# Performance work log

Hardware: AMD Instinct MI355X
Metric: run time of the kernel (lower is better)

Reference implementation:

```python
import jax, jax.numpy as jnp
import numpy as np

B, H, L, D = 4, 16, 8192, 64


def setup_inputs() -> dict:
    key = jax.random.key(0)
    ks = jax.random.split(key, 10)
    q = jax.random.normal(ks[0], (B, H, L, D), dtype=jnp.float32)
    k = jax.random.normal(ks[1], (B, H, L, D), dtype=jnp.float32)
    v = jax.random.normal(ks[2], (B, H, L, D), dtype=jnp.float32)
    mask = jax.random.randint(ks[3], (B, H, L), 0, 2, dtype=jnp.int32)
    s = 1.0 / np.sqrt(D)
    Wa_w = jax.random.uniform(ks[4], (D, D), jnp.float32, -s, s)  # torch Linear weight [out,in]
    Wa_b = jax.random.uniform(ks[5], (D,), jnp.float32, -s, s)
    Ua_w = jax.random.uniform(ks[6], (D, D), jnp.float32, -s, s)
    Ua_b = jax.random.uniform(ks[7], (D,), jnp.float32, -s, s)
    va_w = jax.random.uniform(ks[8], (1, D), jnp.float32, -s, s)
    va_b = jax.random.uniform(ks[9], (1,), jnp.float32, -s, s)
    return {"q": q, "k": k, "v": v, "mask": mask,
            "Wa_w": Wa_w, "Wa_b": Wa_b, "Ua_w": Ua_w, "Ua_b": Ua_b,
            "va_w": va_w, "va_b": va_b}


def reference(q, k, v, mask, Wa_w, Wa_b, Ua_w, Ua_b, va_w, va_b):
    # e1 = Wa(q), e2 = Ua(k)  (torch Linear: x @ W.T + b)
    e1 = jnp.einsum('bhld,ed->bhle', q, Wa_w) + Wa_b
    e2 = jnp.einsum('bhld,ed->bhle', k, Ua_w) + Ua_b
    t = jnp.tanh(e1 + e2)
    # va: [B,H,L,D] -> [B,H,L]
    e = jnp.einsum('bhld,d->bhl', t, va_w[0]) + va_b[0]
    e = jnp.where(mask == 0, jnp.float32(-10000.0), e)
    alpha = jax.nn.softmax(e, axis=-1)  # softmax over sequence length
    return alpha[..., None] * v
```

## Files before the change

### kernel.cpp

```cpp
#include <hip/hip_runtime.h>
#include <hip/hip_bf16.h>

#define BH   64
#define LSEQ 8192
#define DDIM 64
#define NPOS (BH * LSEQ)
#define NT4  (NPOS * DDIM / 4)

typedef __attribute__((ext_vector_type(8))) short bf16x8;
typedef __attribute__((ext_vector_type(4))) float f32x4;

__device__ inline short f2bf(float f) {
    unsigned u = __builtin_bit_cast(unsigned, f);
    unsigned r = (u + 0x7FFFu + ((u >> 16) & 1u)) >> 16;
    return (short)r;
}
__device__ inline float bf2f(short s) {
    unsigned u = ((unsigned)(unsigned short)s) << 16;
    return __builtin_bit_cast(float, u);
}
__device__ inline void split8(const float* f, bf16x8& hi, bf16x8& lo) {
#pragma unroll
    for (int j = 0; j < 8; j++) {
        short h = f2bf(f[j]);
        hi[j] = h;
        lo[j] = f2bf(f[j] - bf2f(h));
    }
}
__device__ inline float tanh_fast(float x) {
    float ex = __expf(2.f * x);
    return 1.f - 2.f * __builtin_amdgcn_rcpf(ex + 1.f);
}

__global__ __launch_bounds__(256) void score_kernel(
    const float* __restrict__ q, const float* __restrict__ k,
    const int*   __restrict__ mask,
    const float* __restrict__ Waw, const float* __restrict__ Wab,
    const float* __restrict__ Uaw, const float* __restrict__ Uab,
    const float* __restrict__ vaw, const float* __restrict__ vab_p,
    float* __restrict__ e_out)
{
    const int lane = threadIdx.x & 63;
    const int m    = lane & 15;
    const int quad = lane >> 4;
    const int wgl  = blockIdx.x * 4 + (threadIdx.x >> 6);
    const long t0  = (long)wgl * 4;

    bf16x8 bwa[4][2], bua[4][2];
    float bias_s[4], vav[4];
#pragma unroll
    for (int t = 0; t < 4; t++) {
        const int n = t * 16 + m;
        bias_s[t] = Wab[n] + Uab[n];
        vav[t]    = vaw[n];
#pragma unroll
        for (int s = 0; s < 2; s++) {
            const int k0 = s * 32 + quad * 8;
            const float4 wA = ((const float4*)(Waw + n * 64 + k0))[0];
            const float4 wB = ((const float4*)(Waw + n * 64 + k0))[1];
            const float4 uA = ((const float4*)(Uaw + n * 64 + k0))[0];
            const float4 uB = ((const float4*)(Uaw + n * 64 + k0))[1];
            float wf[8] = {wA.x, wA.y, wA.z, wA.w, wB.x, wB.y, wB.z, wB.w};
            float uf[8] = {uA.x, uA.y, uA.z, uA.w, uB.x, uB.y, uB.z, uB.w};
            bf16x8 wv, uv;
#pragma unroll
            for (int j = 0; j < 8; j++) { wv[j] = f2bf(wf[j]); uv[j] = f2bf(uf[j]); }
            bwa[t][s] = wv;
            bua[t][s] = uv;
        }
    }
    const float vab = vab_p[0];

    float4 A[8], B[8];
    int4 mkA, mkB;

    auto issue = [&](float4 (&buf)[8], int4& mk, long tile) {
        mk = ((const int4*)mask)[tile * 4 + quad];
        const size_t off = (size_t)(tile * 16 + m) * 64 + quad * 8;
        buf[0] = *((const float4*)(q + off));
        buf[1] = *((const float4*)(q + off + 4));
        buf[2] = *((const float4*)(k + off));
        buf[3] = *((const float4*)(k + off + 4));
        buf[4] = *((const float4*)(q + off + 32));
        buf[5] = *((const float4*)(q + off + 36));
        buf[6] = *((const float4*)(k + off + 32));
        buf[7] = *((const float4*)(k + off + 36));
    };

    auto compute = [&](const float4 (&buf)[8], const int4& mk, long tile) {
        f32x4 acc[4];
#pragma unroll
        for (int t = 0; t < 4; t++) acc[t] = (f32x4){0.f, 0.f, 0.f, 0.f};
#pragma unroll
        for (int s = 0; s < 2; s++) {
            const float4 qa = buf[s * 4 + 0], qb = buf[s * 4 + 1];
            const float4 ka = buf[s * 4 + 2], kb = buf[s * 4 + 3];
            float qf[8] = {qa.x, qa.y, qa.z, qa.w, qb.x, qb.y, qb.z, qb.w};
            float kf[8] = {ka.x, ka.y, ka.z, ka.w, kb.x, kb.y, kb.z, kb.w};
            bf16x8 qhi, qlo, khi, klo;
            split8(qf, qhi, qlo);
            split8(kf, khi, klo);
#pragma unroll
            for (int t = 0; t < 4; t++) {
                acc[t] = __builtin_amdgcn_mfma_f32_16x16x32_bf16(qhi, bwa[t][s], acc[t], 0, 0, 0);
                acc[t] = __builtin_amdgcn_mfma_f32_16x16x32_bf16(qlo, bwa[t][s], acc[t], 0, 0, 0);
                acc[t] = __builtin_amdgcn_mfma_f32_16x16x32_bf16(khi, bua[t][s], acc[t], 0, 0, 0);
                acc[t] = __builtin_amdgcn_mfma_f32_16x16x32_bf16(klo, bua[t][s], acc[t], 0, 0, 0);
            }
        }
        float c[4] = {0.f, 0.f, 0.f, 0.f};
#pragma unroll
        for (int t = 0; t < 4; t++) {
#pragma unroll
            for (int r = 0; r < 4; r++)
                c[r] += vav[t] * tanh_fast(acc[t][r] + bias_s[t]);
        }
#pragma unroll
        for (int r = 0; r < 4; r++) {
#pragma unroll
            for (int off2 = 1; off2 < 16; off2 <<= 1)
                c[r] += __shfl_xor(c[r], off2, 16);
        }
        if (m == 0) {
            float4 ev;
            ev.x = mk.x ? c[0] + vab : -10000.f;
            ev.y = mk.y ? c[1] + vab : -10000.f;
            ev.z = mk.z ? c[2] + vab : -10000.f;
            ev.w = mk.w ? c[3] + vab : -10000.f;
            *((float4*)(e_out + tile * 16 + quad * 4)) = ev;
        }
    };

    issue(A, mkA, t0 + 0);
    issue(B, mkB, t0 + 1);
    compute(A, mkA, t0 + 0);
    issue(A, mkA, t0 + 2);
    compute(B, mkB, t0 + 1);
    issue(B, mkB, t0 + 3);
    compute(A, mkA, t0 + 2);
    compute(B, mkB, t0 + 3);
}

__global__ __launch_bounds__(1024) void rowstat_kernel(
    const float* __restrict__ e, float* __restrict__ stats)
{
    const int row = blockIdx.x;
    const size_t base = (size_t)row * LSEQ;
    const int tid  = threadIdx.x;
    const int lane = tid & 63;
    const int wv   = tid >> 6;
    __shared__ float redmax[16];
    __shared__ float redsum[16];

    float4 e0 = ((const float4*)(e + base))[tid];
    float4 e1 = ((const float4*)(e + base))[1024 + tid];
    float em[8] = {e0.x, e0.y, e0.z, e0.w, e1.x, e1.y, e1.z, e1.w};

    float lm = em[0];
#pragma unroll
    for (int j = 1; j < 8; j++) lm = fmaxf(lm, em[j]);
#pragma unroll
    for (int off = 32; off >= 1; off >>= 1) lm = fmaxf(lm, __shfl_xor(lm, off, 64));
    if (lane == 0) redmax[wv] = lm;
    __syncthreads();
    float M = redmax[0];
#pragma unroll
    for (int i = 1; i < 16; i++) M = fmaxf(M, redmax[i]);

    float ls = 0.f;
#pragma unroll
    for (int j = 0; j < 8; j++) ls += __expf(em[j] - M);
#pragma unroll
    for (int off = 32; off >= 1; off >>= 1) ls += __shfl_xor(ls, off, 64);
    if (lane == 0) redsum[wv] = ls;
    __syncthreads();
    if (tid == 0) {
        float S = 0.f;
#pragma unroll
        for (int i = 0; i < 16; i++) S += redsum[i];
        stats[row * 2]     = M;
        stats[row * 2 + 1] = 1.f / S;
    }
}

__global__ __launch_bounds__(256) void scale_kernel(
    const float* __restrict__ v, const float* __restrict__ e,
    const float* __restrict__ stats, float* __restrict__ out)
{
    const size_t i0 = (size_t)blockIdx.x * 256 + threadIdx.x;
    const size_t i1 = i0 + (size_t)(NT4 / 2);

    float4 v0 = ((const float4*)v)[i0];
    float4 v1 = ((const float4*)v)[i1];
    const size_t p0 = i0 >> 4, p1 = i1 >> 4;
    float e0 = e[p0], e1 = e[p1];
    const size_t r0 = p0 >> 13, r1 = p1 >> 13;
    float M0 = stats[r0 * 2], I0 = stats[r0 * 2 + 1];
    float M1 = stats[r1 * 2], I1 = stats[r1 * 2 + 1];

    float a0 = __expf(e0 - M0) * I0;
    float a1 = __expf(e1 - M1) * I1;
    float4 o0 = make_float4(a0 * v0.x, a0 * v0.y, a0 * v0.z, a0 * v0.w);
    float4 o1 = make_float4(a1 * v1.x, a1 * v1.y, a1 * v1.z, a1 * v1.w);
    ((float4*)out)[i0] = o0;
    ((float4*)out)[i1] = o1;
}

extern "C" void kernel_launch(void* const* d_in, const int* in_sizes, int n_in,
                              void* d_out, int out_size, void* d_ws, size_t ws_size,
                              hipStream_t stream) {
    const float* q    = (const float*)d_in[0];
    const float* k    = (const float*)d_in[1];
    const float* v    = (const float*)d_in[2];
    const int*   mask = (const int*)d_in[3];
    const float* Waw  = (const float*)d_in[4];
    const float* Wab  = (const float*)d_in[5];
    const float* Uaw  = (const float*)d_in[6];
    const float* Uab  = (const float*)d_in[7];
    const float* vaw  = (const float*)d_in[8];
    const float* vab  = (const float*)d_in[9];
    float* out = (float*)d_out;

    float* e_buf = (float*)d_ws;
    float* stats = (float*)d_ws + NPOS;

    score_kernel<<<2048, 256, 0, stream>>>(q, k, mask, Waw, Wab, Uaw, Uab, vaw, vab, e_buf);
    rowstat_kernel<<<BH, 1024, 0, stream>>>(e_buf, stats);
    scale_kernel<<<NT4 / 2 / 256, 256, 0, stream>>>(v, e_buf, stats, out);
}
```

Before: 418.8 us.

## Reorder weight loads after tile prefetch, add occupancy hint, nontemporal scale kernel

```diff
diff --git a/kernel.cpp b/kernel.cpp
--- a/kernel.cpp
+++ b/kernel.cpp
@@ -11,9 +11,8 @@
 typedef __attribute__((ext_vector_type(4))) float f32x4;
 
 __device__ inline short f2bf(float f) {
-    unsigned u = __builtin_bit_cast(unsigned, f);
-    unsigned r = (u + 0x7FFFu + ((u >> 16) & 1u)) >> 16;
-    return (short)r;
+    __bf16 b = (__bf16)f;
+    return __builtin_bit_cast(short, b);
 }
 __device__ inline float bf2f(short s) {
     unsigned u = ((unsigned)(unsigned short)s) << 16;
@@ -32,7 +31,7 @@
     return 1.f - 2.f * __builtin_amdgcn_rcpf(ex + 1.f);
 }
 
-__global__ __launch_bounds__(256) void score_kernel(
+__global__ __launch_bounds__(256, 3) void score_kernel(
     const float* __restrict__ q, const float* __restrict__ k,
     const int*   __restrict__ mask,
     const float* __restrict__ Waw, const float* __restrict__ Wab,
@@ -48,28 +47,7 @@
 
     bf16x8 bwa[4][2], bua[4][2];
     float bias_s[4], vav[4];
-#pragma unroll
-    for (int t = 0; t < 4; t++) {
-        const int n = t * 16 + m;
-        bias_s[t] = Wab[n] + Uab[n];
-        vav[t]    = vaw[n];
-#pragma unroll
-        for (int s = 0; s < 2; s++) {
-            const int k0 = s * 32 + quad * 8;
-            const float4 wA = ((const float4*)(Waw + n * 64 + k0))[0];
-            const float4 wB = ((const float4*)(Waw + n * 64 + k0))[1];
-            const float4 uA = ((const float4*)(Uaw + n * 64 + k0))[0];
-            const float4 uB = ((const float4*)(Uaw + n * 64 + k0))[1];
-            float wf[8] = {wA.x, wA.y, wA.z, wA.w, wB.x, wB.y, wB.z, wB.w};
-            float uf[8] = {uA.x, uA.y, uA.z, uA.w, uB.x, uB.y, uB.z, uB.w};
-            bf16x8 wv, uv;
-#pragma unroll
-            for (int j = 0; j < 8; j++) { wv[j] = f2bf(wf[j]); uv[j] = f2bf(uf[j]); }
-            bwa[t][s] = wv;
-            bua[t][s] = uv;
-        }
-    }
-    const float vab = vab_p[0];
+    float vab;
 
     float4 A[8], B[8];
     int4 mkA, mkB;
@@ -87,6 +65,31 @@
         buf[7] = *((const float4*)(k + off + 36));
     };
 
+    auto load_weights = [&]() {
+#pragma unroll
+        for (int t = 0; t < 4; t++) {
+            const int n = t * 16 + m;
+            bias_s[t] = Wab[n] + Uab[n];
+            vav[t]    = vaw[n];
+#pragma unroll
+            for (int s = 0; s < 2; s++) {
+                const int k0 = s * 32 + quad * 8;
+                const float4 wA = ((const float4*)(Waw + n * 64 + k0))[0];
+                const float4 wB = ((const float4*)(Waw + n * 64 + k0))[1];
+                const float4 uA = ((const float4*)(Uaw + n * 64 + k0))[0];
+                const float4 uB = ((const float4*)(Uaw + n * 64 + k0))[1];
+                float wf[8] = {wA.x, wA.y, wA.z, wA.w, wB.x, wB.y, wB.z, wB.w};
+                float uf[8] = {uA.x, uA.y, uA.z, uA.w, uB.x, uB.y, uB.z, uB.w};
+                bf16x8 wv, uv;
+#pragma unroll
+                for (int j = 0; j < 8; j++) { wv[j] = f2bf(wf[j]); uv[j] = f2bf(uf[j]); }
+                bwa[t][s] = wv;
+                bua[t][s] = uv;
+            }
+        }
+        vab = vab_p[0];
+    };
+
     auto compute = [&](const float4 (&buf)[8], const int4& mk, long tile) {
         f32x4 acc[4];
 #pragma unroll
@@ -133,10 +136,15 @@
 
     issue(A, mkA, t0 + 0);
     issue(B, mkB, t0 + 1);
+    __builtin_amdgcn_sched_barrier(0);
+    load_weights();
+    __builtin_amdgcn_sched_barrier(0);
     compute(A, mkA, t0 + 0);
     issue(A, mkA, t0 + 2);
+    __builtin_amdgcn_sched_barrier(0);
     compute(B, mkB, t0 + 1);
     issue(B, mkB, t0 + 3);
+    __builtin_amdgcn_sched_barrier(0);
     compute(A, mkA, t0 + 2);
     compute(B, mkB, t0 + 3);
 }
@@ -187,23 +195,31 @@
     const float* __restrict__ v, const float* __restrict__ e,
     const float* __restrict__ stats, float* __restrict__ out)
 {
-    const size_t i0 = (size_t)blockIdx.x * 256 + threadIdx.x;
-    const size_t i1 = i0 + (size_t)(NT4 / 2);
-
-    float4 v0 = ((const float4*)v)[i0];
-    float4 v1 = ((const float4*)v)[i1];
-    const size_t p0 = i0 >> 4, p1 = i1 >> 4;
-    float e0 = e[p0], e1 = e[p1];
-    const size_t r0 = p0 >> 13, r1 = p1 >> 13;
-    float M0 = stats[r0 * 2], I0 = stats[r0 * 2 + 1];
-    float M1 = stats[r1 * 2], I1 = stats[r1 * 2 + 1];
-
-    float a0 = __expf(e0 - M0) * I0;
-    float a1 = __expf(e1 - M1) * I1;
-    float4 o0 = make_float4(a0 * v0.x, a0 * v0.y, a0 * v0.z, a0 * v0.w);
-    float4 o1 = make_float4(a1 * v1.x, a1 * v1.y, a1 * v1.z, a1 * v1.w);
-    ((float4*)out)[i0] = o0;
-    ((float4*)out)[i1] = o1;
+    const size_t b0 = (size_t)blockIdx.x * 1024 + threadIdx.x;
+    const f32x4* vp = (const f32x4*)v;
+    f32x4*       op = (f32x4*)out;
+
+    size_t idx[4];
+    f32x4  vv[4];
+    float  ee[4];
+    float2 st[4];
+#pragma unroll
+    for (int j = 0; j < 4; j++) {
+        idx[j] = b0 + (size_t)j * 256;
+        vv[j]  = __builtin_nontemporal_load(vp + idx[j]);
+    }
+#pragma unroll
+    for (int j = 0; j < 4; j++) {
+        const size_t p = idx[j] >> 4;
+        ee[j] = e[p];
+        st[j] = ((const float2*)stats)[p >> 13];
+    }
+#pragma unroll
+    for (int j = 0; j < 4; j++) {
+        const float a = __expf(ee[j] - st[j].x) * st[j].y;
+        f32x4 o = vv[j] * a;
+        __builtin_nontemporal_store(o, op + idx[j]);
+    }
 }
 
 extern "C" void kernel_launch(void* const* d_in, const int* in_sizes, int n_in,
@@ -226,5 +242,5 @@
 
     score_kernel<<<2048, 256, 0, stream>>>(q, k, mask, Waw, Wab, Uaw, Uab, vaw, vab, e_buf);
     rowstat_kernel<<<BH, 1024, 0, stream>>>(e_buf, stats);
-    scale_kernel<<<NT4 / 2 / 256, 256, 0, stream>>>(v, e_buf, stats, out);
-}
+    scale_kernel<<<NT4 / 1024, 256, 0, stream>>>(v, e_buf, stats, out);
+}
```

Result: no change. 423.9 us (+1.2%).
